# Kernel tuning notes

Hardware: AMD Instinct MI355X
Metric: run time of the kernel (lower is better)

Reference implementation:

```python
import jax, jax.numpy as jnp
import numpy as np

PASSES = 6
S = 2           # numEdgeSets
D = 256         # inputLayerSize
OUT = 10        # outputLayerSize
HID = 80
B, N, E = 4, 10000, 160000


def _leaky(x):
    return jax.nn.leaky_relu(x, negative_slope=0.01)


def setup_inputs() -> dict:
    key = jax.random.key(0)
    ks = jax.random.split(key, 18)
    sc = 0.05
    return {
        "nodes": jax.random.normal(ks[0], (B, N, D), jnp.float32),
        "edges": jax.random.randint(ks[1], (B, S, E, 2), 0, N, jnp.int32),
        "problem_type": jax.random.uniform(ks[2], (B, 1), jnp.float32),
        # GRUCell params (torch layout: [3D, D] for ih and hh)
        "gru_w_ih": jax.random.normal(ks[3], (3 * D, D), jnp.float32) * sc,
        "gru_w_hh": jax.random.normal(ks[4], (3 * D, D), jnp.float32) * sc,
        "gru_b_ih": jax.random.normal(ks[5], (3 * D,), jnp.float32) * sc,
        "gru_b_hh": jax.random.normal(ks[6], (3 * D,), jnp.float32) * sc,
        # per-edge-set 2-layer MLP, stacked over edge sets
        "edge_w1": jax.random.normal(ks[7], (S, D, D), jnp.float32) * sc,
        "edge_b1": jax.random.normal(ks[8], (S, D), jnp.float32) * sc,
        "edge_w2": jax.random.normal(ks[9], (S, D, D), jnp.float32) * sc,
        "edge_b2": jax.random.normal(ks[10], (S, D), jnp.float32) * sc,
        # readout head
        "fc1_w": jax.random.normal(ks[11], (HID, D + 1), jnp.float32) * sc,
        "fc1_b": jax.random.normal(ks[12], (HID,), jnp.float32) * sc,
        "fc2_w": jax.random.normal(ks[13], (HID, HID), jnp.float32) * sc,
        "fc2_b": jax.random.normal(ks[14], (HID,), jnp.float32) * sc,
        "fc3_w": jax.random.normal(ks[15], (OUT, HID), jnp.float32) * sc,
        "fc3_b": jax.random.normal(ks[16], (OUT,), jnp.float32) * sc,
    }


def _gru_cell(x, h, w_ih, w_hh, b_ih, b_hh):
    # torch.nn.GRUCell semantics; x,h: [B,N,D]
    gi = jnp.einsum("bnd,ed->bne", x, w_ih) + b_ih   # [B,N,3D]
    gh = jnp.einsum("bnd,ed->bne", h, w_hh) + b_hh
    i_r, i_z, i_n = jnp.split(gi, 3, axis=-1)
    h_r, h_z, h_n = jnp.split(gh, 3, axis=-1)
    r = jax.nn.sigmoid(i_r + h_r)
    z = jax.nn.sigmoid(i_z + h_z)
    n = jnp.tanh(i_n + r * h_n)
    return (1.0 - z) * n + z * h


def reference(nodes, edges, problem_type, gru_w_ih, gru_w_hh, gru_b_ih, gru_b_hh,
              edge_w1, edge_b1, edge_w2, edge_b2,
              fc1_w, fc1_b, fc2_w, fc2_b, fc3_w, fc3_b):
    bidx = jnp.arange(B)[:, None]  # [B,1] for batched scatter
    h = nodes
    for j in range(PASSES):
        incoming = jnp.zeros_like(h)
        for si in range(S):
            dst = edges[:, si, :, 0]  # [B,E]
            src = edges[:, si, :, 1]  # [B,E]
            gathered = jnp.take_along_axis(h, src[:, :, None], axis=1)  # [B,E,D]
            y = _leaky(jnp.einsum("bed,fd->bef", gathered, edge_w1[si]) + edge_b1[si])
            y = jnp.einsum("bed,fd->bef", y, edge_w2[si]) + edge_b2[si]
            incoming = incoming.at[bidx, dst].add(y)
        h = _gru_cell(incoming, h, gru_w_ih, gru_w_hh, gru_b_ih, gru_b_hh)
        if j < PASSES - 2:
            h = jax.lax.stop_gradient(h)  # mirrors .detach()
    # graph readout: sum over nodes, log, nan->0, relu, +inf->finite max
    s = jnp.sum(h, axis=1)               # [B,D]
    l = jnp.log(s)
    l = jnp.where(jnp.isnan(l), 0.0, l)
    l = jax.nn.relu(l)
    finite_max = jnp.max(jnp.where(jnp.isinf(l), -jnp.inf, l), axis=1, keepdims=True)
    l = jnp.where(jnp.isinf(l), finite_max, l)
    x = jnp.concatenate([l, problem_type], axis=1)  # [B,D+1]
    x = _leaky(x @ fc1_w.T + fc1_b)
    x = _leaky(x @ fc2_w.T + fc2_b)
    return x @ fc3_w.T + fc3_b  # [B,OUT]
```

## Files before the change

### kernel.cpp

```cpp
#include <hip/hip_runtime.h>
#include <math.h>

#define NNODES 10000
#define NEDGES 160000
#define DIM    256
#define BATCH  4
#define NG     8
#define MROWS  40064
#define RBLK   625
#define RGRP   79
#define RBLK128 313
#define RGRP128 40

typedef __attribute__((ext_vector_type(8))) __bf16 bf16x8;
typedef __attribute__((ext_vector_type(4))) float  floatx4;
typedef __attribute__((ext_vector_type(8))) unsigned short ushort8v;

__device__ __forceinline__ float leakyf(float x){ return x > 0.f ? x : 0.01f*x; }
__device__ __forceinline__ float fsig(float x){ return 1.f/(1.f + __expf(-x)); }
__device__ __forceinline__ float ftanh(float x){ return 1.f - 2.f/(1.f + __expf(2.f*x)); }
__device__ __forceinline__ unsigned short f2bf_u(float x){
  unsigned int u = __float_as_uint(x);
  u += 0x7fffu + ((u >> 16) & 1u);
  return (unsigned short)(u >> 16);
}
__device__ __forceinline__ float bfdec(unsigned short u){
  return __uint_as_float(((unsigned int)u) << 16);
}
#define GATE_SCL 65535.f
#define GATE_INV 1.5259021896696422e-5f

__device__ __forceinline__ void glds16(unsigned short* lds, const unsigned short* g){
  __builtin_amdgcn_global_load_lds(
      (const __attribute__((address_space(1))) void*)g,
      (__attribute__((address_space(3))) void*)lds, 16, 0, 0);
}

__global__ void ihinit_kernel(const float* __restrict__ nodes,
                              unsigned short* __restrict__ ihcat,
                              unsigned short* __restrict__ h_lo){
  int idx = blockIdx.x*256 + threadIdx.x;
  int row = idx >> 8, d = idx & 255;
  float v = nodes[idx];
  unsigned short h = f2bf_u(v);
  ihcat[(size_t)row*512 + 256 + d] = h;
  h_lo[idx] = f2bf_u(v - bfdec(h));
}

__global__ void w1cat_kernel(const float* __restrict__ ew1, unsigned short* __restrict__ o){
  int idx = blockIdx.x*256 + threadIdx.x;
  int n = idx >> 8, k = idx & 255;
  o[idx] = f2bf_u(ew1[(n>>8)*65536 + (n&255)*256 + k]);
}
__global__ void w2k_kernel(const float* __restrict__ ew2, unsigned short* __restrict__ o){
  int idx = blockIdx.x*256 + threadIdx.x;
  int n = idx >> 10, kp = idx & 1023;
  int j = kp & 511, term = kp >> 9;
  int si = j >> 8, k = j & 255;
  float v = ew2[si*65536 + n*256 + k];
  unsigned short h = f2bf_u(v);
  o[idx] = term ? f2bf_u(v - bfdec(h)) : h;
}
__global__ void wk2_kernel(const float* __restrict__ w, unsigned short* __restrict__ o){
  int idx = blockIdx.x*256 + threadIdx.x;
  int c = idx >> 9, kp = idx & 511;
  int k = kp & 255, term = kp >> 8;
  float v = w[c*256 + k];
  unsigned short h = f2bf_u(v);
  o[idx] = term ? f2bf_u(v - bfdec(h)) : h;
}
__global__ void wcomb_kernel(const float* __restrict__ wih, const float* __restrict__ whh,
                             unsigned short* __restrict__ o){
  int idx = blockIdx.x*256 + threadIdx.x;
  int c = idx >> 10, kp = idx & 1023;
  int seg = kp >> 8, k = kp & 255;
  const float* w = (seg & 1) ? whh : wih;
  float v = w[c*256 + k];
  unsigned short h = f2bf_u(v);
  o[idx] = (seg >> 1) ? f2bf_u(v - bfdec(h)) : h;
}

__global__ void hist_kernel(const int* __restrict__ edges, int* __restrict__ cnt){
  int idx = blockIdx.x*256 + threadIdx.x;
  if (idx < NG*NEDGES){
    int g = idx / NEDGES, e = idx - g*NEDGES;
    int d = edges[((size_t)g*NEDGES + e)*2];
    atomicAdd(&cnt[g*NNODES + d], 1);
  }
}

__global__ __launch_bounds__(256) void scan_kernel(const int* __restrict__ cnt, int* __restrict__ off){
  __shared__ int sc[256];
  int g = blockIdx.x, t = threadIdx.x;
  int base = 0;
  for (int c=0;c<40;c++){
    int i = c*256 + t;
    int v = (i < NNODES) ? cnt[g*NNODES + i] : 0;
    __syncthreads();
    sc[t] = v;
    __syncthreads();
    for (int o=1;o<256;o<<=1){
      int u = (t>=o) ? sc[t-o] : 0;
      __syncthreads();
      sc[t] += u;
      __syncthreads();
    }
    if (i < NNODES) off[g*(NNODES+1) + i] = base + sc[t] - v;
    base += sc[255];
  }
  if (t == 0) off[g*(NNODES+1) + NNODES] = base;
}

__global__ void scatter_kernel(const int* __restrict__ edges, const int* __restrict__ off,
                               int* __restrict__ cur, int* __restrict__ ssrc){
  int idx = blockIdx.x*256 + threadIdx.x;
  if (idx < NG*NEDGES){
    int g = idx / NEDGES, e = idx - g*NEDGES;
    const int* ep = &edges[((size_t)g*NEDGES + e)*2];
    int d = ep[0], s = ep[1];
    int pos = off[g*(NNODES+1) + d] + atomicAdd(&cur[g*NNODES + d], 1);
    ssrc[g*NEDGES + pos] = s;
  }
}

template<int KP, int RS, int KM>
__device__ __forceinline__ void mm64_core(
    const unsigned short* __restrict__ Ab, const unsigned short* __restrict__ Wb,
    unsigned short* lds, floatx4 (&acc)[4][2])
{
  const int t = threadIdx.x;
  const int w = t >> 6, lane = t & 63;
  const int q = lane >> 4, col = lane & 15;
  const int wc = w*32;
  unsigned short* Al = lds;
  unsigned short* Bl = lds + 64*64;

  const int sr = t >> 3;
  const int sj = t & 7;
  const int sk = ((sj ^ (sr & 7)) * 8);

  for (int kb = 0; kb < KP; kb += 64){
    #pragma unroll
    for (int i=0;i<2;i++){
      int r = i*32 + sr;
      glds16(&Al[i*2048 + w*512], &Ab[(size_t)r*RS + ((kb + sk) & KM)]);
    }
    #pragma unroll
    for (int i=0;i<4;i++){
      int r = i*32 + sr;
      glds16(&Bl[i*2048 + w*512], &Wb[(size_t)r*KP + kb + sk]);
    }
    __syncthreads();
    #pragma unroll
    for (int ks2=0; ks2<2; ks2++){
      bf16x8 a[4], bf[2];
      #pragma unroll
      for (int mi=0;mi<4;mi++){
        int r = mi*16 + col;
        int j = (ks2*4 + q) ^ (r & 7);
        a[mi] = *(const bf16x8*)&Al[r*64 + j*8];
      }
      #pragma unroll
      for (int ni=0;ni<2;ni++){
        int r = wc + ni*16 + col;
        int j = (ks2*4 + q) ^ (r & 7);
        bf[ni] = *(const bf16x8*)&Bl[r*64 + j*8];
      }
      #pragma unroll
      for (int mi=0;mi<4;mi++)
        #pragma unroll
        for (int ni=0;ni<2;ni++)
          acc[mi][ni] = __builtin_amdgcn_mfma_f32_16x16x32_bf16(a[mi], bf[ni], acc[mi][ni], 0,0,0);
    }
    __syncthreads();
  }
}

template<int KP, int RS, int KM>
__device__ __forceinline__ void mm128_core(
    const unsigned short* __restrict__ Ab, const unsigned short* __restrict__ Wb,
    unsigned short* lds, floatx4 (&acc)[4][4])
{
  const int t = threadIdx.x;
  const int w = t >> 6, lane = t & 63;
  const int q = lane >> 4, col = lane & 15;
  const int wr = (w >> 1) * 64;
  const int wc = (w & 1) * 64;
  unsigned short* Al = lds;
  unsigned short* Bl = lds + 128*64;

  const int sr = t >> 3;
  const int sj = t & 7;
  const int sk = ((sj ^ (sr & 7)) * 8);

  for (int kb = 0; kb < KP; kb += 64){
    #pragma unroll
    for (int i=0;i<4;i++){
      int r = i*32 + sr;
      glds16(&Al[i*2048 + w*512], &Ab[(size_t)r*RS + ((kb + sk) & KM)]);
      glds16(&Bl[i*2048 + w*512], &Wb[(size_t)r*KP + kb + sk]);
    }
    __syncthreads();
    #pragma unroll
    for (int ks2=0; ks2<2; ks2++){
      bf16x8 a[4], bf[4];
      #pragma unroll
      for (int mi=0;mi<4;mi++){
        int r = wr + mi*16 + col;
        int j = (ks2*4 + q) ^ (r & 7);
        a[mi] = *(const bf16x8*)&Al[r*64 + j*8];
      }
      #pragma unroll
      for (int ni=0;ni<4;ni++){
        int r = wc + ni*16 + col;
        int j = (ks2*4 + q) ^ (r & 7);
        bf[ni] = *(const bf16x8*)&Bl[r*64 + j*8];
      }
      #pragma unroll
      for (int mi=0;mi<4;mi++)
        #pragma unroll
        for (int ni=0;ni<4;ni++)
          acc[mi][ni] = __builtin_amdgcn_mfma_f32_16x16x32_bf16(a[mi], bf[ni], acc[mi][ni], 0,0,0);
    }
    __syncthreads();
  }
}

#define XDECODE(NCOL) \
  const int bid_ = blockIdx.x; \
  const int rb_ = ((bid_ >> 3) / NCOL) * 8 + (bid_ & 7); \
  const int colb_ = (bid_ >> 3) % NCOL; \
  if (rb_ >= RBLK) return;

#define XDECODE128(NCOL) \
  const int bid_ = blockIdx.x; \
  const int rb_ = ((bid_ >> 3) / NCOL) * 8 + (bid_ & 7); \
  const int colb_ = (bid_ >> 3) % NCOL; \
  if (rb_ >= RBLK128) return;

#define MMPRO \
  const int t = threadIdx.x, w = t >> 6, lane = t & 63; \
  const int q = lane >> 4, col = lane & 15; \
  const int wc = w*32; \
  floatx4 acc[4][2]; \
  _Pragma("unroll") for (int mi=0;mi<4;mi++) _Pragma("unroll") for (int ni=0;ni<2;ni++) \
    acc[mi][ni] = (floatx4){0.f,0.f,0.f,0.f};

#define MMPRO128 \
  const int t = threadIdx.x, w = t >> 6, lane = t & 63; \
  const int q = lane >> 4, col = lane & 15; \
  const int wrq = (w >> 1) * 64, wcq = (w & 1) * 64; \
  floatx4 acc[4][4]; \
  _Pragma("unroll") for (int mi=0;mi<4;mi++) _Pragma("unroll") for (int ni=0;ni<4;ni++) \
    acc[mi][ni] = (floatx4){0.f,0.f,0.f,0.f};

__global__ __launch_bounds__(256) void z64_kernel(
    const unsigned short* __restrict__ ihcat, const unsigned short* __restrict__ w1cat,
    const float* __restrict__ eb1, unsigned short* __restrict__ Z)
{
  __shared__ unsigned short lds[16384];
  XDECODE128(4)
  const int row0 = rb_*128, col0 = colb_*128;
  MMPRO128
  mm128_core<256,512,255>(ihcat + (size_t)row0*512 + 256, w1cat + (size_t)col0*256, lds, acc);

  #pragma unroll
  for (int ni=0;ni<4;ni++){
    int n = col0 + wcq + ni*16 + col;
    int si = n >> 8, cz = n & 255;
    float bb = eb1[si*256 + cz];
    unsigned short* zp = Z + (size_t)si*MROWS*256 + cz;
    #pragma unroll
    for (int mi=0;mi<4;mi++)
      #pragma unroll
      for (int rr=0;rr<4;rr++){
        int row = row0 + wrq + mi*16 + q*4 + rr;
        zp[(size_t)row*256] = f2bf_u(leakyf(acc[mi][ni][rr] + bb));
      }
  }
}

__global__ __launch_bounds__(256) void aggregate_kernel(
    const unsigned short* __restrict__ Z, const int* __restrict__ ssrc,
    const int* __restrict__ off, unsigned short* __restrict__ Sb)
{
  const int bid = blockIdx.x;
  const int g = bid & 7;
  const int dgrp = bid >> 3;
  const int b = g >> 1, si = g & 1;
  const int w = threadIdx.x >> 6, lane = threadIdx.x & 63;
  const int half = lane >> 5, c = lane & 31;
  const unsigned short* zb = Z + ((size_t)si*MROWS + b*10000)*256 + c*8;
  const int* sp = ssrc + (size_t)g*NEDGES;
  const int* offg = off + g*(NNODES+1);

  #pragma unroll
  for (int p=0;p<2;p++){
    const int d = dgrp*16 + w*4 + p*2 + half;
    int j = offg[d];
    const int j1 = offg[d+1];
    float a0=0.f,a1=0.f,a2=0.f,a3=0.f,a4=0.f,a5=0.f,a6=0.f,a7=0.f;
    for (; j+4 <= j1; j+=4){
      int s0=sp[j], s1=sp[j+1], s2=sp[j+2], s3=sp[j+3];
      ushort8v u0 = *(const ushort8v*)&zb[(size_t)s0*256];
      ushort8v u1 = *(const ushort8v*)&zb[(size_t)s1*256];
      ushort8v u2 = *(const ushort8v*)&zb[(size_t)s2*256];
      ushort8v u3 = *(const ushort8v*)&zb[(size_t)s3*256];
      a0 += bfdec(u0[0])+bfdec(u1[0])+bfdec(u2[0])+bfdec(u3[0]);
      a1 += bfdec(u0[1])+bfdec(u1[1])+bfdec(u2[1])+bfdec(u3[1]);
      a2 += bfdec(u0[2])+bfdec(u1[2])+bfdec(u2[2])+bfdec(u3[2]);
      a3 += bfdec(u0[3])+bfdec(u1[3])+bfdec(u2[3])+bfdec(u3[3]);
      a4 += bfdec(u0[4])+bfdec(u1[4])+bfdec(u2[4])+bfdec(u3[4]);
      a5 += bfdec(u0[5])+bfdec(u1[5])+bfdec(u2[5])+bfdec(u3[5]);
      a6 += bfdec(u0[6])+bfdec(u1[6])+bfdec(u2[6])+bfdec(u3[6]);
      a7 += bfdec(u0[7])+bfdec(u1[7])+bfdec(u2[7])+bfdec(u3[7]);
    }
    for (; j < j1; j++){
      ushort8v u = *(const ushort8v*)&zb[(size_t)sp[j]*256];
      a0+=bfdec(u[0]); a1+=bfdec(u[1]); a2+=bfdec(u[2]); a3+=bfdec(u[3]);
      a4+=bfdec(u[4]); a5+=bfdec(u[5]); a6+=bfdec(u[6]); a7+=bfdec(u[7]);
    }
    size_t so = (size_t)(b*10000 + d)*512 + si*256 + c*8;
    ushort8v hv;
    hv[0]=f2bf_u(a0); hv[1]=f2bf_u(a1); hv[2]=f2bf_u(a2); hv[3]=f2bf_u(a3);
    hv[4]=f2bf_u(a4); hv[5]=f2bf_u(a5); hv[6]=f2bf_u(a6); hv[7]=f2bf_u(a7);
    *(ushort8v*)&Sb[so] = hv;
  }
}

__global__ __launch_bounds__(256) void w264_kernel(
    const unsigned short* __restrict__ Sb, const unsigned short* __restrict__ w2k,
    const float* __restrict__ eb2, const int* __restrict__ off,
    unsigned short* __restrict__ ihcat)
{
  __shared__ unsigned short lds[16384];
  XDECODE128(2)
  const int row0 = rb_*128, col0 = colb_*128;
  MMPRO128
  mm128_core<1024,512,511>(Sb + (size_t)row0*512, w2k + (size_t)col0*1024, lds, acc);

  float b20[4], b21[4];
  #pragma unroll
  for (int ni=0;ni<4;ni++){
    int n = col0 + wcq + ni*16 + col;
    b20[ni] = eb2[n];
    b21[ni] = eb2[256 + n];
  }
  #pragma unroll
  for (int mi=0;mi<4;mi++)
    #pragma unroll
    for (int rr=0;rr<4;rr++){
      int row = row0 + wrq + mi*16 + q*4 + rr;
      int rw = (row < 40000) ? row : 39999;
      int b = rw / 10000, d = rw - b*10000;
      int o0 = (b*2)*(NNODES+1) + d;
      int o1 = (b*2+1)*(NNODES+1) + d;
      float dg0 = (float)(off[o0+1] - off[o0]);
      float dg1 = (float)(off[o1+1] - off[o1]);
      #pragma unroll
      for (int ni=0;ni<4;ni++){
        int n = col0 + wcq + ni*16 + col;
        ihcat[(size_t)row*512 + n] = f2bf_u(acc[mi][ni][rr] + dg0*b20[ni] + dg1*b21[ni]);
      }
    }
}

__global__ __launch_bounds__(256) void gruA_kernel(
    const unsigned short* __restrict__ ihcat, const unsigned short* __restrict__ wcomb,
    const float* __restrict__ b_ih, const float* __restrict__ b_hh,
    unsigned short* __restrict__ rz_r, unsigned short* __restrict__ rz_z)
{
  __shared__ unsigned short lds[16384];
  XDECODE128(4)
  const int row0 = rb_*128, col0 = colb_*128;
  MMPRO128
  mm128_core<1024,512,511>(ihcat + (size_t)row0*512, wcomb + (size_t)col0*1024, lds, acc);

  float bb[4];
  #pragma unroll
  for (int ni=0;ni<4;ni++){
    int n = col0 + wcq + ni*16 + col;
    bb[ni] = b_ih[n] + b_hh[n];
  }
  unsigned short* dst = (col0 < 256) ? rz_r : rz_z;
  const int cbase = (col0 & 255) + wcq;
  #pragma unroll
  for (int mi=0;mi<4;mi++)
    #pragma unroll
    for (int rr=0;rr<4;rr++){
      size_t row = (size_t)(row0 + wrq + mi*16 + q*4 + rr);
      #pragma unroll
      for (int ni=0;ni<4;ni++){
        float v = fsig(acc[mi][ni][rr] + bb[ni]);
        dst[row*256 + cbase + ni*16 + col] = (unsigned short)(v*GATE_SCL + 0.5f);
      }
    }
}

__global__ __launch_bounds__(256) void gruB_kernel(
    const unsigned short* __restrict__ ihcat, unsigned short* __restrict__ h_lo,
    const unsigned short* __restrict__ wihk, const unsigned short* __restrict__ whhk,
    const float* __restrict__ b_ih, const float* __restrict__ b_hh,
    const unsigned short* __restrict__ rz_r, const unsigned short* __restrict__ rz_z,
    unsigned short* __restrict__ ihcat_nxt)
{
  __shared__ unsigned short lds[12288];
  XDECODE(2)
  const int row0 = rb_*64, dcol0 = colb_*128;
  const int t = threadIdx.x, w = t >> 6, lane = t & 63;
  const int q = lane >> 4, col = lane & 15;
  const int wc = w*32;

  floatx4 ai[4][2], ah[4][2];
  #pragma unroll
  for (int mi=0;mi<4;mi++)
    #pragma unroll
    for (int ni=0;ni<2;ni++){ ai[mi][ni] = (floatx4){0.f,0.f,0.f,0.f}; ah[mi][ni] = (floatx4){0.f,0.f,0.f,0.f}; }

  mm64_core<512,512,255>(ihcat + (size_t)row0*512,       wihk + (size_t)(512 + dcol0)*512, lds, ai);
  mm64_core<512,512,255>(ihcat + (size_t)row0*512 + 256, whhk + (size_t)(512 + dcol0)*512, lds, ah);

  float bi[2], bh[2];
  #pragma unroll
  for (int ni=0;ni<2;ni++){
    int n = 512 + dcol0 + wc + ni*16 + col;
    bi[ni] = b_ih[n]; bh[ni] = b_hh[n];
  }
  #pragma unroll
  for (int mi=0;mi<4;mi++)
    #pragma unroll
    for (int rr=0;rr<4;rr++){
      size_t row = (size_t)(row0 + mi*16 + q*4 + rr);
      #pragma unroll
      for (int ni=0;ni<2;ni++){
        int dn = dcol0 + wc + ni*16 + col;
        float rg = (float)rz_r[row*256 + dn] * GATE_INV;
        float zg = (float)rz_z[row*256 + dn] * GATE_INV;
        float ng = ftanh(ai[mi][ni][rr] + bi[ni] + rg*(ah[mi][ni][rr] + bh[ni]));
        float hv = bfdec(ihcat[row*512 + 256 + dn]) + bfdec(h_lo[row*256 + dn]);
        float hnew = (1.f - zg)*ng + zg*hv;
        unsigned short hh = f2bf_u(hnew);
        ihcat_nxt[row*512 + 256 + dn] = hh;
        h_lo[row*256 + dn] = f2bf_u(hnew - bfdec(hh));
      }
    }
}

__global__ void reduce_kernel(const unsigned short* __restrict__ ihcat,
                              const unsigned short* __restrict__ h_lo,
                              float* __restrict__ sbuf){
  int b  = blockIdx.x / 50;
  int s0 = (blockIdx.x % 50) * 200;
  int d  = threadIdx.x;
  size_t row = (size_t)b*NNODES + s0;
  float acc = 0.f;
  for (int i=0;i<200;i++){
    acc += bfdec(ihcat[(row+i)*512 + 256 + d]) + bfdec(h_lo[(row+i)*256 + d]);
  }
  atomicAdd(&sbuf[b*DIM + d], acc);
}

__global__ __launch_bounds__(320) void head_kernel(
    const float* __restrict__ sbuf, const float* __restrict__ pt,
    const float* __restrict__ fc1w, const float* __restrict__ fc1b,
    const float* __restrict__ fc2w, const float* __restrict__ fc2b,
    const float* __restrict__ fc3w, const float* __restrict__ fc3b,
    float* __restrict__ out)
{
  __shared__ float L[4][257];
  __shared__ float T1[4][80];
  __shared__ float T2[4][80];
  __shared__ float fmx[4];
  int t = threadIdx.x;
  if (t < 256){
    for (int b=0;b<4;b++){
      float v = sbuf[b*DIM + t];
      float ll = logf(v);
      if (ll != ll) ll = 0.f;
      ll = fmaxf(ll, 0.f);
      L[b][t] = ll;
    }
  }
  __syncthreads();
  int w = t >> 6, lane = t & 63;
  if (w < 4){
    float m = -INFINITY;
    for (int i=lane;i<256;i+=64){ float v = L[w][i]; if (v != INFINITY) m = fmaxf(m, v); }
    #pragma unroll
    for (int o=32;o>=1;o>>=1) m = fmaxf(m, __shfl_xor(m, o, 64));
    if (lane==0) fmx[w] = m;
  }
  __syncthreads();
  if (t < 256){
    for (int b=0;b<4;b++) if (L[b][t] == INFINITY) L[b][t] = fmx[b];
  }
  if (t < 4) L[t][256] = pt[t];
  __syncthreads();
  if (t < 320){
    int b = t/80, i = t%80;
    float a = fc1b[i];
    for (int k=0;k<257;k++) a += L[b][k]*fc1w[i*257+k];
    T1[b][i] = leakyf(a);
  }
  __syncthreads();
  if (t < 320){
    int b = t/80, i = t%80;
    float a = fc2b[i];
    for (int k=0;k<80;k++) a += T1[b][k]*fc2w[i*80+k];
    T2[b][i] = leakyf(a);
  }
  __syncthreads();
  if (t < 40){
    int b = t/10, i = t%10;
    float a = fc3b[i];
    for (int k=0;k<80;k++) a += T2[b][k]*fc3w[i*80+k];
    out[b*10+i] = a;
  }
}

extern "C" void kernel_launch(void* const* d_in, const int* in_sizes, int n_in,
                              void* d_out, int out_size, void* d_ws, size_t ws_size,
                              hipStream_t stream) {
  const float* nodes = (const float*)d_in[0];
  const int*   edges = (const int*)d_in[1];
  const float* pt    = (const float*)d_in[2];
  const float* w_ih  = (const float*)d_in[3];
  const float* w_hh  = (const float*)d_in[4];
  const float* b_ih  = (const float*)d_in[5];
  const float* b_hh  = (const float*)d_in[6];
  const float* ew1   = (const float*)d_in[7];
  const float* eb1   = (const float*)d_in[8];
  const float* ew2   = (const float*)d_in[9];
  const float* eb2   = (const float*)d_in[10];
  const float* fc1w  = (const float*)d_in[11];
  const float* fc1b  = (const float*)d_in[12];
  const float* fc2w  = (const float*)d_in[13];
  const float* fc2b  = (const float*)d_in[14];
  const float* fc3w  = (const float*)d_in[15];
  const float* fc3b  = (const float*)d_in[16];

  const size_t HN  = (size_t)BATCH*NNODES*DIM;
  const size_t HNP = (size_t)MROWS*DIM;
  char* p = (char*)d_ws;
  float* sbuf = (float*)p;                        p += BATCH*DIM*4;
  unsigned short* ihcat0 = (unsigned short*)p;    p += (size_t)MROWS*512*2;
  unsigned short* ihcat1 = (unsigned short*)p;    p += (size_t)MROWS*512*2;
  unsigned short* h_lo   = (unsigned short*)p;    p += HNP*2;
  unsigned short* Zb   = (unsigned short*)p;      p += 2*HNP*2;
  unsigned short* Sb   = (unsigned short*)p;      p += (size_t)MROWS*512*2;
  unsigned short* w1cat= (unsigned short*)p;      p += 512*256*2;
  unsigned short* w2k  = (unsigned short*)p;      p += 256*1024*2;
  unsigned short* wihk = (unsigned short*)p;      p += 768*512*2;
  unsigned short* whhk = (unsigned short*)p;      p += 768*512*2;
  unsigned short* wcomb= (unsigned short*)p;      p += 512*1024*2;
  int* off  = (int*)p;                            p += NG*(NNODES+1)*4;
  int* cur  = (int*)p;                            p += NG*NNODES*4;
  int* ssrc = (int*)p;                            p += (size_t)NG*NEDGES*4;

  unsigned short* rz_r = (unsigned short*)Sb;
  unsigned short* rz_z = rz_r + (size_t)MROWS*256;

  w1cat_kernel<<<512,256,0,stream>>>(ew1, w1cat);
  w2k_kernel<<<1024,256,0,stream>>>(ew2, w2k);
  wk2_kernel<<<1536,256,0,stream>>>(w_ih, wihk);
  wk2_kernel<<<1536,256,0,stream>>>(w_hh, whhk);
  wcomb_kernel<<<2048,256,0,stream>>>(w_ih, w_hh, wcomb);

  ihinit_kernel<<<(int)(HN/256),256,0,stream>>>(nodes, ihcat0, h_lo);

  hipMemsetAsync(cur, 0, NG*NNODES*sizeof(int), stream);
  hist_kernel<<<(NG*NEDGES)/256,256,0,stream>>>(edges, cur);
  scan_kernel<<<NG,256,0,stream>>>(cur, off);
  hipMemsetAsync(cur, 0, NG*NNODES*sizeof(int), stream);
  scatter_kernel<<<(NG*NEDGES)/256,256,0,stream>>>(edges, off, cur, ssrc);

  hipMemsetAsync(sbuf, 0, BATCH*DIM*sizeof(float), stream);

  unsigned short* ih[2] = {ihcat0, ihcat1};

  for (int pass=0; pass<6; pass++){
    unsigned short* curb = ih[pass & 1];
    unsigned short* nxtb = ih[(pass+1) & 1];
    z64_kernel<<<RGRP128*8*4,256,0,stream>>>(curb, w1cat, eb1, Zb);
    aggregate_kernel<<<5000,256,0,stream>>>(Zb, ssrc, off, Sb);
    w264_kernel<<<RGRP128*8*2,256,0,stream>>>(Sb, w2k, eb2, off, curb);
    gruA_kernel<<<RGRP128*8*4,256,0,stream>>>(curb, wcomb, b_ih, b_hh, rz_r, rz_z);
    gruB_kernel<<<RGRP*8*2,256,0,stream>>>(curb, h_lo, wihk, whhk, b_ih, b_hh,
                                           rz_r, rz_z, nxtb);
  }
  reduce_kernel<<<200,256,0,stream>>>(ih[0], h_lo, sbuf);
  head_kernel<<<1,320,0,stream>>>(sbuf, pt, fc1w,fc1b,fc2w,fc2b,fc3w,fc3b,(float*)d_out);
}
```

Measured before the change: 1.723 ms.

## Double-buffer LDS tiles in GEMM cores and unroll edge gather by eight

Both mm64_core and mm128_core now ping-pong between two LDS buffers, issuing the global-to-LDS loads for the next K slice before the MFMA work on the current one, so load latency overlaps compute. The GEMM kernels' shared memory doubles to hold both buffers, which may reduce occupancy. The edge aggregation kernel also gains an 8-wide unrolled loop that issues eight row gathers before accumulating, to expose more memory-level parallelism. Correctness relies on the single trailing barrier per iteration separating writes to one buffer from reads of the other.

```diff
diff --git a/kernel.cpp b/kernel.cpp
--- a/kernel.cpp
+++ b/kernel.cpp
@@ -132,25 +132,45 @@
   const int w = t >> 6, lane = t & 63;
   const int q = lane >> 4, col = lane & 15;
   const int wc = w*32;
-  unsigned short* Al = lds;
-  unsigned short* Bl = lds + 64*64;
 
   const int sr = t >> 3;
   const int sj = t & 7;
   const int sk = ((sj ^ (sr & 7)) * 8);
 
-  for (int kb = 0; kb < KP; kb += 64){
+  {
+    unsigned short* Al = lds;
+    unsigned short* Bl = lds + 4096;
     #pragma unroll
     for (int i=0;i<2;i++){
       int r = i*32 + sr;
-      glds16(&Al[i*2048 + w*512], &Ab[(size_t)r*RS + ((kb + sk) & KM)]);
+      glds16(&Al[i*2048 + w*512], &Ab[(size_t)r*RS + (sk & KM)]);
     }
     #pragma unroll
     for (int i=0;i<4;i++){
       int r = i*32 + sr;
-      glds16(&Bl[i*2048 + w*512], &Wb[(size_t)r*KP + kb + sk]);
-    }
-    __syncthreads();
+      glds16(&Bl[i*2048 + w*512], &Wb[(size_t)r*KP + sk]);
+    }
+  }
+  __syncthreads();
+  int cur = 0;
+  for (int kb = 0; kb < KP; kb += 64){
+    if (kb + 64 < KP){
+      unsigned short* Al = lds + (cur^1)*12288;
+      unsigned short* Bl = Al + 4096;
+      int kn = kb + 64;
+      #pragma unroll
+      for (int i=0;i<2;i++){
+        int r = i*32 + sr;
+        glds16(&Al[i*2048 + w*512], &Ab[(size_t)r*RS + ((kn + sk) & KM)]);
+      }
+      #pragma unroll
+      for (int i=0;i<4;i++){
+        int r = i*32 + sr;
+        glds16(&Bl[i*2048 + w*512], &Wb[(size_t)r*KP + kn + sk]);
+      }
+    }
+    const unsigned short* Al = lds + cur*12288;
+    const unsigned short* Bl = Al + 4096;
     #pragma unroll
     for (int ks2=0; ks2<2; ks2++){
       bf16x8 a[4], bf[2];
@@ -173,6 +193,7 @@
           acc[mi][ni] = __builtin_amdgcn_mfma_f32_16x16x32_bf16(a[mi], bf[ni], acc[mi][ni], 0,0,0);
     }
     __syncthreads();
+    cur ^= 1;
   }
 }
 
@@ -186,21 +207,37 @@
   const int q = lane >> 4, col = lane & 15;
   const int wr = (w >> 1) * 64;
   const int wc = (w & 1) * 64;
-  unsigned short* Al = lds;
-  unsigned short* Bl = lds + 128*64;
 
   const int sr = t >> 3;
   const int sj = t & 7;
   const int sk = ((sj ^ (sr & 7)) * 8);
 
-  for (int kb = 0; kb < KP; kb += 64){
+  {
+    unsigned short* Al = lds;
+    unsigned short* Bl = lds + 8192;
     #pragma unroll
     for (int i=0;i<4;i++){
       int r = i*32 + sr;
-      glds16(&Al[i*2048 + w*512], &Ab[(size_t)r*RS + ((kb + sk) & KM)]);
-      glds16(&Bl[i*2048 + w*512], &Wb[(size_t)r*KP + kb + sk]);
-    }
-    __syncthreads();
+      glds16(&Al[i*2048 + w*512], &Ab[(size_t)r*RS + (sk & KM)]);
+      glds16(&Bl[i*2048 + w*512], &Wb[(size_t)r*KP + sk]);
+    }
+  }
+  __syncthreads();
+  int cur = 0;
+  for (int kb = 0; kb < KP; kb += 64){
+    if (kb + 64 < KP){
+      unsigned short* Al = lds + (cur^1)*16384;
+      unsigned short* Bl = Al + 8192;
+      int kn = kb + 64;
+      #pragma unroll
+      for (int i=0;i<4;i++){
+        int r = i*32 + sr;
+        glds16(&Al[i*2048 + w*512], &Ab[(size_t)r*RS + ((kn + sk) & KM)]);
+        glds16(&Bl[i*2048 + w*512], &Wb[(size_t)r*KP + kn + sk]);
+      }
+    }
+    const unsigned short* Al = lds + cur*16384;
+    const unsigned short* Bl = Al + 8192;
     #pragma unroll
     for (int ks2=0; ks2<2; ks2++){
       bf16x8 a[4], bf[4];
@@ -223,6 +260,7 @@
           acc[mi][ni] = __builtin_amdgcn_mfma_f32_16x16x32_bf16(a[mi], bf[ni], acc[mi][ni], 0,0,0);
     }
     __syncthreads();
+    cur ^= 1;
   }
 }
 
@@ -258,7 +296,7 @@
     const unsigned short* __restrict__ ihcat, const unsigned short* __restrict__ w1cat,
     const float* __restrict__ eb1, unsigned short* __restrict__ Z)
 {
-  __shared__ unsigned short lds[16384];
+  __shared__ unsigned short lds[32768];
   XDECODE128(4)
   const int row0 = rb_*128, col0 = colb_*128;
   MMPRO128
@@ -300,6 +338,30 @@
     int j = offg[d];
     const int j1 = offg[d+1];
     float a0=0.f,a1=0.f,a2=0.f,a3=0.f,a4=0.f,a5=0.f,a6=0.f,a7=0.f;
+    for (; j+8 <= j1; j+=8){
+      int s[8];
+      #pragma unroll
+      for (int e=0;e<8;e++) s[e] = sp[j+e];
+      ushort8v u[8];
+      #pragma unroll
+      for (int e=0;e<8;e++) u[e] = *(const ushort8v*)&zb[(size_t)s[e]*256];
+      a0 += bfdec(u[0][0])+bfdec(u[1][0])+bfdec(u[2][0])+bfdec(u[3][0]);
+      a1 += bfdec(u[0][1])+bfdec(u[1][1])+bfdec(u[2][1])+bfdec(u[3][1]);
+      a2 += bfdec(u[0][2])+bfdec(u[1][2])+bfdec(u[2][2])+bfdec(u[3][2]);
+      a3 += bfdec(u[0][3])+bfdec(u[1][3])+bfdec(u[2][3])+bfdec(u[3][3]);
+      a4 += bfdec(u[0][4])+bfdec(u[1][4])+bfdec(u[2][4])+bfdec(u[3][4]);
+      a5 += bfdec(u[0][5])+bfdec(u[1][5])+bfdec(u[2][5])+bfdec(u[3][5]);
+      a6 += bfdec(u[0][6])+bfdec(u[1][6])+bfdec(u[2][6])+bfdec(u[3][6]);
+      a7 += bfdec(u[0][7])+bfdec(u[1][7])+bfdec(u[2][7])+bfdec(u[3][7]);
+      a0 += bfdec(u[4][0])+bfdec(u[5][0])+bfdec(u[6][0])+bfdec(u[7][0]);
+      a1 += bfdec(u[4][1])+bfdec(u[5][1])+bfdec(u[6][1])+bfdec(u[7][1]);
+      a2 += bfdec(u[4][2])+bfdec(u[5][2])+bfdec(u[6][2])+bfdec(u[7][2]);
+      a3 += bfdec(u[4][3])+bfdec(u[5][3])+bfdec(u[6][3])+bfdec(u[7][3]);
+      a4 += bfdec(u[4][4])+bfdec(u[5][4])+bfdec(u[6][4])+bfdec(u[7][4]);
+      a5 += bfdec(u[4][5])+bfdec(u[5][5])+bfdec(u[6][5])+bfdec(u[7][5]);
+      a6 += bfdec(u[4][6])+bfdec(u[5][6])+bfdec(u[6][6])+bfdec(u[7][6]);
+      a7 += bfdec(u[4][7])+bfdec(u[5][7])+bfdec(u[6][7])+bfdec(u[7][7]);
+    }
     for (; j+4 <= j1; j+=4){
       int s0=sp[j], s1=sp[j+1], s2=sp[j+2], s3=sp[j+3];
       ushort8v u0 = *(const ushort8v*)&zb[(size_t)s0*256];
@@ -333,7 +395,7 @@
     const float* __restrict__ eb2, const int* __restrict__ off,
     unsigned short* __restrict__ ihcat)
 {
-  __shared__ unsigned short lds[16384];
+  __shared__ unsigned short lds[32768];
   XDECODE128(2)
   const int row0 = rb_*128, col0 = colb_*128;
   MMPRO128
@@ -370,7 +432,7 @@
     const float* __restrict__ b_ih, const float* __restrict__ b_hh,
     unsigned short* __restrict__ rz_r, unsigned short* __restrict__ rz_z)
 {
-  __shared__ unsigned short lds[16384];
+  __shared__ unsigned short lds[32768];
   XDECODE128(4)
   const int row0 = rb_*128, col0 = colb_*128;
   MMPRO128
@@ -404,7 +466,7 @@
     const unsigned short* __restrict__ rz_r, const unsigned short* __restrict__ rz_z,
     unsigned short* __restrict__ ihcat_nxt)
 {
-  __shared__ unsigned short lds[12288];
+  __shared__ unsigned short lds[24576];
   XDECODE(2)
   const int row0 = rb_*64, dcol0 = colb_*128;
   const int t = threadIdx.x, w = t >> 6, lane = t & 63;
```

Measured after the change: 1.702 ms. No clear change (-1.2%).
